# Kernel tuning notes

Measured on AMD Instinct MI355X. Metric: run time of the kernel, lower is better.

The kernel has to match this reference:

```python
import jax, jax.numpy as jnp
import numpy as np

N_SRC = 50000
N_DST = 50000
N_EDGES = 800000
D = 128
H = 128


def setup_inputs() -> dict:
    key = jax.random.key(0)
    ks = jax.random.split(key, 10)
    return {
        "feat_src": jax.random.normal(ks[0], (N_SRC, D), dtype=jnp.float32),
        "feat_dst": jax.random.normal(ks[1], (N_DST, D), dtype=jnp.float32),
        "W1": jax.random.normal(ks[2], (H, D), dtype=jnp.float32) * 0.05,
        "b1": jnp.zeros((H,), dtype=jnp.float32),
        "W2": jax.random.normal(ks[3], (H, 3 * D), dtype=jnp.float32) * 0.05,
        "b2": jnp.zeros((H,), dtype=jnp.float32),
        "W3": jax.random.normal(ks[4], (H, 2 * H), dtype=jnp.float32) * 0.05,
        "b3": jnp.zeros((H,), dtype=jnp.float32),
        "src_idx": jax.random.randint(ks[5], (N_EDGES,), 0, N_SRC, dtype=jnp.int32),
        "dst_idx": jax.random.randint(ks[6], (N_EDGES,), 0, N_DST, dtype=jnp.int32),
    }


def reference(feat_src, feat_dst, W1, b1, W2, b2, W3, b3, src_idx, dst_idx):
    n_dst = feat_dst.shape[0]
    # copy_u: gather source features along edges  [E, D]
    m = feat_src[src_idx]
    # fn.max -> 'max'; NOTE: source code's 'mean' is ALSO fn.max (faithful to bug)
    mx = jax.ops.segment_max(m, dst_idx, num_segments=n_dst)
    mx = jnp.where(jnp.isfinite(mx), mx, jnp.zeros_like(mx))  # zero-degree dst -> 0 (DGL convention)
    sm = jax.ops.segment_sum(m, dst_idx, num_segments=n_dst)
    agg = jnp.concatenate([mx, mx, sm], axis=1)  # [N_dst, 3D]
    z2 = agg @ W2.T + b2            # fc2
    z1 = feat_dst @ W1.T + b1       # fc1
    h = jax.nn.relu(jnp.concatenate([z2, z1], axis=1))  # [N_dst, 2H]
    out = jax.nn.relu(h @ W3.T + b3)  # fc3 = Linear + ReLU
    return out
```

## Files before the change

kernel.cpp:

```cpp
#include <hip/hip_runtime.h>
#include <math.h>

#define NDST 50000
#define NSRC 50000
#define NEDGE 800000
#define DF 128

#define NBUK 1563
#define NCH 128
#define EPC (NEDGE / NCH)
#define HN (NBUK * NCH)
#define CAP 1536

typedef __attribute__((ext_vector_type(4))) float f32x4;
typedef __attribute__((ext_vector_type(8))) short bf16x8;

__device__ __forceinline__ ushort f2bf(float f) {
    union { float f; unsigned int u; } c; c.f = f;
    unsigned int u = c.u;
    unsigned int r = (u + 0x7fffu + ((u >> 16) & 1u)) >> 16;
    return (ushort)r;
}
__device__ __forceinline__ float bflo(unsigned int u) {
    union { unsigned int u; float f; } c; c.u = u << 16; return c.f;
}
__device__ __forceinline__ float bfhi(unsigned int u) {
    union { unsigned int u; float f; } c; c.u = u & 0xffff0000u; return c.f;
}

#define NB_CONV 6250
#define NB_CONVD 6250
#define NB_ZERO 196
#define NB_WF 40

__global__ void prep_all(const float* __restrict__ fs, unsigned int* __restrict__ fs_b,
                         const float* __restrict__ fd, unsigned int* __restrict__ fd_b,
                         uint4* __restrict__ hist4,
                         const float* __restrict__ W2, const float* __restrict__ W1,
                         const float* __restrict__ W3,
                         ushort* __restrict__ Wzf, ushort* __restrict__ W1f,
                         ushort* __restrict__ W3f) {
    int b = blockIdx.x, tid = threadIdx.x;
    if (b < NB_CONV + NB_CONVD) {
        const float* src = (b < NB_CONV) ? fs : fd;
        unsigned int* dst = (b < NB_CONV) ? fs_b : fd_b;
        int i = ((b < NB_CONV) ? b : b - NB_CONV) * 256 + tid;
        float4 v = *(const float4*)(src + (size_t)i * 4);
        unsigned int lo = (unsigned int)f2bf(v.x) | ((unsigned int)f2bf(v.y) << 16);
        unsigned int hi = (unsigned int)f2bf(v.z) | ((unsigned int)f2bf(v.w) << 16);
        *(uint2*)(dst + (size_t)i * 2) = make_uint2(lo, hi);
    } else if (b < NB_CONV + NB_CONVD + NB_ZERO) {
        int i = (b - NB_CONV - NB_CONVD) * 256 + tid;
        if (i < HN / 4) hist4[i] = make_uint4(0, 0, 0, 0);
    } else {
        int i = (b - NB_CONV - NB_CONVD - NB_ZERO) * 256 + tid;
        float v[8];
        ushort* outp;
        if (i < 4096) {
            int e = i, lane = e & 63, nt = (e >> 6) & 7, ks = e >> 9;
            int n = nt * 16 + (lane & 15), kb = ks * 32 + ((lane >> 4) << 3);
            #pragma unroll
            for (int j = 0; j < 8; ++j) {
                int col = kb + j;
                v[j] = (col < 128) ? (W2[n * 384 + col] + W2[n * 384 + 128 + col])
                                   : W2[n * 384 + 128 + col];
            }
            outp = Wzf + (size_t)e * 8;
        } else if (i < 4096 + 2048) {
            int e = i - 4096, lane = e & 63, nt = (e >> 6) & 7, ks = e >> 9;
            int n = nt * 16 + (lane & 15), kb = ks * 32 + ((lane >> 4) << 3);
            #pragma unroll
            for (int j = 0; j < 8; ++j) v[j] = W1[n * 128 + kb + j];
            outp = W1f + (size_t)e * 8;
        } else if (i < 4096 + 2048 + 4096) {
            int e = i - 6144, lane = e & 63, nt = (e >> 6) & 7, ks = e >> 9;
            int n = nt * 16 + (lane & 15), kb = ks * 32 + ((lane >> 4) << 3);
            #pragma unroll
            for (int j = 0; j < 8; ++j) v[j] = W3[n * 256 + kb + j];
            outp = W3f + (size_t)e * 8;
        } else return;
        unsigned int u0 = (unsigned int)f2bf(v[0]) | ((unsigned int)f2bf(v[1]) << 16);
        unsigned int u1 = (unsigned int)f2bf(v[2]) | ((unsigned int)f2bf(v[3]) << 16);
        unsigned int u2 = (unsigned int)f2bf(v[4]) | ((unsigned int)f2bf(v[5]) << 16);
        unsigned int u3 = (unsigned int)f2bf(v[6]) | ((unsigned int)f2bf(v[7]) << 16);
        *(uint4*)outp = make_uint4(u0, u1, u2, u3);
    }
}

__global__ void hist_k(const int* __restrict__ dst_idx, int* __restrict__ hist) {
    int c = blockIdx.x, tid = threadIdx.x;
    int base = c * EPC;
    for (int e = base + tid; e < base + EPC; e += 256)
        atomicAdd(&hist[(dst_idx[e] >> 5) * NCH + c], 1);
}

__global__ void scan_bsums(const int* __restrict__ a, int* __restrict__ bsum, int n) {
    __shared__ int ws[4];
    int i = blockIdx.x * 256 + threadIdx.x;
    int v = (i < n) ? a[i] : 0;
    #pragma unroll
    for (int off = 32; off > 0; off >>= 1) v += __shfl_down(v, off, 64);
    if ((threadIdx.x & 63) == 0) ws[threadIdx.x >> 6] = v;
    __syncthreads();
    if (threadIdx.x == 0) bsum[blockIdx.x] = ws[0] + ws[1] + ws[2] + ws[3];
}

__global__ __launch_bounds__(256)
void scan_mid(const int* __restrict__ bsum, int* __restrict__ bpre, int nb) {
    __shared__ int part[256];
    int t = threadIdx.x;
    int ch = (nb + 255) / 256;
    int lo = t * ch, hi = min(nb, lo + ch);
    int s = 0;
    for (int i = lo; i < hi; ++i) s += bsum[i];
    part[t] = s;
    __syncthreads();
    for (int off = 1; off < 256; off <<= 1) {
        int v = (t >= off) ? part[t - off] : 0;
        __syncthreads();
        part[t] += v;
        __syncthreads();
    }
    int run = (t == 0) ? 0 : part[t - 1];
    for (int i = lo; i < hi; ++i) { bpre[i] = run; run += bsum[i]; }
}

__global__ __launch_bounds__(256)
void scan_final(const int* __restrict__ a, const int* __restrict__ bpre,
                int* __restrict__ out, int n) {
    __shared__ int s[256];
    int b = blockIdx.x, t = threadIdx.x;
    int i = b * 256 + t;
    int v = (i < n) ? a[i] : 0;
    s[t] = v;
    __syncthreads();
    for (int off = 1; off < 256; off <<= 1) {
        int u = (t >= off) ? s[t - off] : 0;
        __syncthreads();
        s[t] += u;
        __syncthreads();
    }
    if (i < n) out[i] = bpre[b] + s[t] - v;
}

__global__ __launch_bounds__(256)
void partition_k(const int* __restrict__ src_idx, const int* __restrict__ dst_idx,
                 const int* __restrict__ scanned, unsigned int* __restrict__ pairs) {
    __shared__ int offs_l[NBUK];
    int c = blockIdx.x, tid = threadIdx.x;
    for (int i = tid; i < NBUK; i += 256) offs_l[i] = scanned[i * NCH + c];
    __syncthreads();
    int base = c * EPC;
    for (int e = base + tid; e < base + EPC; e += 256) {
        int d = dst_idx[e];
        int pos = atomicAdd(&offs_l[d >> 5], 1);
        pairs[pos] = (unsigned int)src_idx[e] | ((unsigned int)(d & 31) << 16);
    }
}

__global__ __launch_bounds__(256)
void bucket_sort_agg(const unsigned int* __restrict__ fs_b,
                     const unsigned int* __restrict__ pairs,
                     const int* __restrict__ scanned,
                     unsigned int* __restrict__ mx_b, unsigned int* __restrict__ sm_b) {
    __shared__ int s_src[CAP];
    __shared__ int s_cnt[32], s_off[32], s_cur[32];
    int B = blockIdx.x, tid = threadIdx.x;
    int w = tid >> 6, lane = tid & 63;
    int s0 = scanned[B * NCH];
    int s1 = (B + 1 < NBUK) ? scanned[(B + 1) * NCH] : NEDGE;

    float mx0[8], mx1[8], sm0[8], sm1[8];
    #pragma unroll
    for (int j = 0; j < 8; ++j) {
        mx0[j] = -INFINITY; mx1[j] = -INFINITY; sm0[j] = 0.f; sm1[j] = 0.f;
    }

    for (int cs = s0; cs < s1; cs += CAP) {
        int n = min(CAP, s1 - cs);
        if (tid < 32) s_cnt[tid] = 0;
        __syncthreads();
        for (int i = tid; i < n; i += 256)
            atomicAdd(&s_cnt[(pairs[cs + i] >> 16) & 31u], 1);
        __syncthreads();
        if (tid < 32) {
            int v = s_cnt[tid];
            int incl = v;
            #pragma unroll
            for (int d = 1; d < 32; d <<= 1) {
                int o = __shfl_up(incl, d, 64);
                if (tid >= d) incl += o;
            }
            s_off[tid] = incl - v;
            s_cur[tid] = incl - v;
        }
        __syncthreads();
        for (int i = tid; i < n; i += 256) {
            unsigned int p = pairs[cs + i];
            int pos = atomicAdd(&s_cur[(p >> 16) & 31u], 1);
            s_src[pos] = (int)(p & 0xFFFFu);
        }
        __syncthreads();
        #pragma unroll
        for (int j = 0; j < 8; ++j) {
            int dl = w * 8 + j;
            int e = s_off[dl], eend = e + s_cnt[dl];
            for (; e + 3 < eend; e += 4) {
                int i0 = s_src[e], i1 = s_src[e + 1], i2 = s_src[e + 2], i3 = s_src[e + 3];
                unsigned int u0 = fs_b[(size_t)i0 * 64 + lane];
                unsigned int u1 = fs_b[(size_t)i1 * 64 + lane];
                unsigned int u2 = fs_b[(size_t)i2 * 64 + lane];
                unsigned int u3 = fs_b[(size_t)i3 * 64 + lane];
                float a0 = bflo(u0), c0 = bfhi(u0);
                float a1 = bflo(u1), c1 = bfhi(u1);
                float a2 = bflo(u2), c2 = bfhi(u2);
                float a3 = bflo(u3), c3 = bfhi(u3);
                mx0[j] = fmaxf(fmaxf(fmaxf(mx0[j], a0), a1), fmaxf(a2, a3));
                mx1[j] = fmaxf(fmaxf(fmaxf(mx1[j], c0), c1), fmaxf(c2, c3));
                sm0[j] += (a0 + a1) + (a2 + a3);
                sm1[j] += (c0 + c1) + (c2 + c3);
            }
            for (; e < eend; ++e) {
                unsigned int u = fs_b[(size_t)s_src[e] * 64 + lane];
                float a = bflo(u), c = bfhi(u);
                mx0[j] = fmaxf(mx0[j], a);
                mx1[j] = fmaxf(mx1[j], c);
                sm0[j] += a;
                sm1[j] += c;
            }
        }
        __syncthreads();
    }

    int base_d = B * 32;
    #pragma unroll
    for (int j = 0; j < 8; ++j) {
        int d = base_d + w * 8 + j;
        if (d >= NDST) continue;
        float m0 = mx0[j], m1 = mx1[j];
        if (m0 == -INFINITY) m0 = 0.f;
        if (m1 == -INFINITY) m1 = 0.f;
        union { float f; unsigned int u; } c0, c1;
        c0.f = m0; c1.f = m1;
        size_t o = (size_t)d * 64 + lane;
        mx_b[o] = (c0.u >> 16) | (c1.u & 0xFFFF0000u);
        sm_b[o] = (unsigned int)f2bf(sm0[j]) | ((unsigned int)f2bf(sm1[j]) << 16);
    }
}

#define BM2 64
#define LDH 260

__global__ __launch_bounds__(256)
void mlp_fused(const ushort* __restrict__ mxa, const ushort* __restrict__ sma,
               const ushort* __restrict__ fdb,
               const ushort* __restrict__ Wzf, const ushort* __restrict__ W1f,
               const ushort* __restrict__ W3f,
               const float* __restrict__ b1, const float* __restrict__ b2,
               const float* __restrict__ b3,
               float* __restrict__ out) {
    __shared__ ushort Hs[BM2 * LDH];
    int tid = threadIdx.x;
    int bm = blockIdx.x * BM2;
    int wid = tid >> 6, lane = tid & 63;
    int wm = (wid & 1) * 32, wn = (wid >> 1) * 64;
    int lrow = lane & 15, lk8 = (lane >> 4) * 8;
    int rbase = (lane >> 4) * 4;
    int nt0 = (wid >> 1) * 4;

    int am0 = min(bm + wm + lrow, NDST - 1);
    int am1 = min(bm + wm + 16 + lrow, NDST - 1);
    int bn[4];
    #pragma unroll
    for (int ni = 0; ni < 4; ++ni) bn[ni] = wn + ni * 16 + lrow;

    f32x4 acc[2][4];

    bf16x8 A0[8], A1[8];
    #pragma unroll
    for (int k = 0; k < 8; ++k) {
        const ushort* ap = (k < 4) ? mxa : sma;
        int kl = ((k * 32) & 127) + lk8;
        A0[k] = *(const bf16x8*)(ap + (size_t)am0 * 128 + kl);
        A1[k] = *(const bf16x8*)(ap + (size_t)am1 * 128 + kl);
    }
    #pragma unroll
    for (int i = 0; i < 2; ++i)
        #pragma unroll
        for (int j = 0; j < 4; ++j) acc[i][j] = (f32x4){0.f, 0.f, 0.f, 0.f};
    #pragma unroll
    for (int k = 0; k < 8; ++k) {
        #pragma unroll
        for (int ni = 0; ni < 4; ++ni) {
            bf16x8 bf = *(const bf16x8*)(Wzf + ((size_t)((k * 8) + nt0 + ni) * 64 + lane) * 8);
            acc[0][ni] = __builtin_amdgcn_mfma_f32_16x16x32_bf16(A0[k], bf, acc[0][ni], 0, 0, 0);
            acc[1][ni] = __builtin_amdgcn_mfma_f32_16x16x32_bf16(A1[k], bf, acc[1][ni], 0, 0, 0);
        }
    }
    #pragma unroll
    for (int ni = 0; ni < 4; ++ni) {
        float bv = b2[bn[ni]];
        #pragma unroll
        for (int mi = 0; mi < 2; ++mi)
            #pragma unroll
            for (int r = 0; r < 4; ++r)
                Hs[(wm + mi * 16 + rbase + r) * LDH + bn[ni]] =
                    f2bf(fmaxf(acc[mi][ni][r] + bv, 0.f));
    }

    bf16x8 B0[4], B1[4];
    #pragma unroll
    for (int k = 0; k < 4; ++k) {
        int kl = k * 32 + lk8;
        B0[k] = *(const bf16x8*)(fdb + (size_t)am0 * 128 + kl);
        B1[k] = *(const bf16x8*)(fdb + (size_t)am1 * 128 + kl);
    }
    #pragma unroll
    for (int i = 0; i < 2; ++i)
        #pragma unroll
        for (int j = 0; j < 4; ++j) acc[i][j] = (f32x4){0.f, 0.f, 0.f, 0.f};
    #pragma unroll
    for (int k = 0; k < 4; ++k) {
        #pragma unroll
        for (int ni = 0; ni < 4; ++ni) {
            bf16x8 bf = *(const bf16x8*)(W1f + ((size_t)((k * 8) + nt0 + ni) * 64 + lane) * 8);
            acc[0][ni] = __builtin_amdgcn_mfma_f32_16x16x32_bf16(B0[k], bf, acc[0][ni], 0, 0, 0);
            acc[1][ni] = __builtin_amdgcn_mfma_f32_16x16x32_bf16(B1[k], bf, acc[1][ni], 0, 0, 0);
        }
    }
    #pragma unroll
    for (int ni = 0; ni < 4; ++ni) {
        float bv = b1[bn[ni]];
        #pragma unroll
        for (int mi = 0; mi < 2; ++mi)
            #pragma unroll
            for (int r = 0; r < 4; ++r)
                Hs[(wm + mi * 16 + rbase + r) * LDH + 128 + bn[ni]] =
                    f2bf(fmaxf(acc[mi][ni][r] + bv, 0.f));
    }

    __syncthreads();

    #pragma unroll
    for (int i = 0; i < 2; ++i)
        #pragma unroll
        for (int j = 0; j < 4; ++j) acc[i][j] = (f32x4){0.f, 0.f, 0.f, 0.f};
    #pragma unroll
    for (int k = 0; k < 8; ++k) {
        bf16x8 af0 = *(const bf16x8*)&Hs[(wm + lrow) * LDH + k * 32 + lk8];
        bf16x8 af1 = *(const bf16x8*)&Hs[(wm + 16 + lrow) * LDH + k * 32 + lk8];
        #pragma unroll
        for (int ni = 0; ni < 4; ++ni) {
            bf16x8 bf = *(const bf16x8*)(W3f + ((size_t)((k * 8) + nt0 + ni) * 64 + lane) * 8);
            acc[0][ni] = __builtin_amdgcn_mfma_f32_16x16x32_bf16(af0, bf, acc[0][ni], 0, 0, 0);
            acc[1][ni] = __builtin_amdgcn_mfma_f32_16x16x32_bf16(af1, bf, acc[1][ni], 0, 0, 0);
        }
    }
    #pragma unroll
    for (int ni = 0; ni < 4; ++ni) {
        float bv = b3[bn[ni]];
        #pragma unroll
        for (int mi = 0; mi < 2; ++mi)
            #pragma unroll
            for (int r = 0; r < 4; ++r) {
                int m = bm + wm + mi * 16 + rbase + r;
                if (m < NDST)
                    out[(size_t)m * 128 + bn[ni]] = fmaxf(acc[mi][ni][r] + bv, 0.f);
            }
    }
}

extern "C" void kernel_launch(void* const* d_in, const int* in_sizes, int n_in,
                              void* d_out, int out_size, void* d_ws, size_t ws_size,
                              hipStream_t stream) {
    const float* feat_src = (const float*)d_in[0];
    const float* feat_dst = (const float*)d_in[1];
    const float* W1 = (const float*)d_in[2];
    const float* b1 = (const float*)d_in[3];
    const float* W2 = (const float*)d_in[4];
    const float* b2 = (const float*)d_in[5];
    const float* W3 = (const float*)d_in[6];
    const float* b3 = (const float*)d_in[7];
    const int* src_idx = (const int*)d_in[8];
    const int* dst_idx = (const int*)d_in[9];

    float* out = (float*)d_out;

    unsigned int* fs_b = (unsigned int*)d_ws;
    unsigned int* mx_b = fs_b + (size_t)NSRC * 64;
    unsigned int* sm_b = mx_b + (size_t)NDST * 64;
    unsigned int* fd_b = sm_b + (size_t)NDST * 64;
    ushort* Wzf = (ushort*)(fd_b + (size_t)NDST * 64);
    ushort* W1f = Wzf + 128 * 256;
    ushort* W3f = W1f + 128 * 128;
    int* hist    = (int*)(W3f + 128 * 256);
    int* scanned = hist + HN;
    int* bsum    = scanned + HN;
    int* bpre    = bsum + 1024;
    unsigned int* pairs = (unsigned int*)(bpre + 1024);

    const int NBH = (HN + 255) / 256;

    prep_all<<<NB_CONV + NB_CONVD + NB_ZERO + NB_WF, 256, 0, stream>>>(
        feat_src, fs_b, feat_dst, fd_b, (uint4*)hist, W2, W1, W3, Wzf, W1f, W3f);

    hist_k<<<NCH, 256, 0, stream>>>(dst_idx, hist);
    scan_bsums<<<NBH, 256, 0, stream>>>(hist, bsum, HN);
    scan_mid<<<1, 256, 0, stream>>>(bsum, bpre, NBH);
    scan_final<<<NBH, 256, 0, stream>>>(hist, bpre, scanned, HN);
    partition_k<<<NCH, 256, 0, stream>>>(src_idx, dst_idx, scanned, pairs);

    bucket_sort_agg<<<NBUK, 256, 0, stream>>>(fs_b, pairs, scanned, mx_b, sm_b);

    mlp_fused<<<(NDST + BM2 - 1) / BM2, 256, 0, stream>>>(
        (const ushort*)mx_b, (const ushort*)sm_b, (const ushort*)fd_b,
        Wzf, W1f, W3f, b1, b2, b3, out);
}
```

Measured before the change: 170.1 us.

## Give each wave its own 16-row strip in fused MLP, removing block sync

The fused MLP kernel now gives each wavefront its own 16 destination rows across all 128 output columns, instead of having four waves share a 64-row tile split into 32x64 pieces. Each wave writes its hidden activations to a private LDS slice, so the block-wide barrier goes away and the padded stride changes to 264. The trade-off is that A operands are loaded once per wave rather than reused across two row sub-tiles. Each wave also reads the full weight matrices, roughly doubling weight traffic per output row through L2.

```diff
diff --git a/kernel.cpp b/kernel.cpp
--- a/kernel.cpp
+++ b/kernel.cpp
@@ -248,8 +248,7 @@
     }
 }
 
-#define BM2 64
-#define LDH 260
+#define LDH 264
 
 __global__ __launch_bounds__(256)
 void mlp_fused(const ushort* __restrict__ mxa, const ushort* __restrict__ sma,
@@ -259,114 +258,83 @@
                const float* __restrict__ b1, const float* __restrict__ b2,
                const float* __restrict__ b3,
                float* __restrict__ out) {
-    __shared__ ushort Hs[BM2 * LDH];
+    __shared__ ushort Hs[4][16 * LDH];
     int tid = threadIdx.x;
-    int bm = blockIdx.x * BM2;
     int wid = tid >> 6, lane = tid & 63;
-    int wm = (wid & 1) * 32, wn = (wid >> 1) * 64;
-    int lrow = lane & 15, lk8 = (lane >> 4) * 8;
+    int mb = (blockIdx.x * 4 + wid) * 16;
+    if (mb >= NDST) return;
+    ushort* hs = &Hs[wid][0];
+
+    int frow = lane & 15;
+    int fk8 = (lane >> 4) * 8;
     int rbase = (lane >> 4) * 4;
-    int nt0 = (wid >> 1) * 4;
-
-    int am0 = min(bm + wm + lrow, NDST - 1);
-    int am1 = min(bm + wm + 16 + lrow, NDST - 1);
-    int bn[4];
-    #pragma unroll
-    for (int ni = 0; ni < 4; ++ni) bn[ni] = wn + ni * 16 + lrow;
-
-    f32x4 acc[2][4];
-
-    bf16x8 A0[8], A1[8];
+
+    f32x4 acc[8];
+
+    bf16x8 A[8];
     #pragma unroll
     for (int k = 0; k < 8; ++k) {
         const ushort* ap = (k < 4) ? mxa : sma;
-        int kl = ((k * 32) & 127) + lk8;
-        A0[k] = *(const bf16x8*)(ap + (size_t)am0 * 128 + kl);
-        A1[k] = *(const bf16x8*)(ap + (size_t)am1 * 128 + kl);
-    }
-    #pragma unroll
-    for (int i = 0; i < 2; ++i)
-        #pragma unroll
-        for (int j = 0; j < 4; ++j) acc[i][j] = (f32x4){0.f, 0.f, 0.f, 0.f};
-    #pragma unroll
-    for (int k = 0; k < 8; ++k) {
-        #pragma unroll
-        for (int ni = 0; ni < 4; ++ni) {
-            bf16x8 bf = *(const bf16x8*)(Wzf + ((size_t)((k * 8) + nt0 + ni) * 64 + lane) * 8);
-            acc[0][ni] = __builtin_amdgcn_mfma_f32_16x16x32_bf16(A0[k], bf, acc[0][ni], 0, 0, 0);
-            acc[1][ni] = __builtin_amdgcn_mfma_f32_16x16x32_bf16(A1[k], bf, acc[1][ni], 0, 0, 0);
-        }
-    }
-    #pragma unroll
-    for (int ni = 0; ni < 4; ++ni) {
-        float bv = b2[bn[ni]];
-        #pragma unroll
-        for (int mi = 0; mi < 2; ++mi)
-            #pragma unroll
-            for (int r = 0; r < 4; ++r)
-                Hs[(wm + mi * 16 + rbase + r) * LDH + bn[ni]] =
-                    f2bf(fmaxf(acc[mi][ni][r] + bv, 0.f));
-    }
-
-    bf16x8 B0[4], B1[4];
-    #pragma unroll
-    for (int k = 0; k < 4; ++k) {
-        int kl = k * 32 + lk8;
-        B0[k] = *(const bf16x8*)(fdb + (size_t)am0 * 128 + kl);
-        B1[k] = *(const bf16x8*)(fdb + (size_t)am1 * 128 + kl);
-    }
-    #pragma unroll
-    for (int i = 0; i < 2; ++i)
-        #pragma unroll
-        for (int j = 0; j < 4; ++j) acc[i][j] = (f32x4){0.f, 0.f, 0.f, 0.f};
-    #pragma unroll
-    for (int k = 0; k < 4; ++k) {
-        #pragma unroll
-        for (int ni = 0; ni < 4; ++ni) {
-            bf16x8 bf = *(const bf16x8*)(W1f + ((size_t)((k * 8) + nt0 + ni) * 64 + lane) * 8);
-            acc[0][ni] = __builtin_amdgcn_mfma_f32_16x16x32_bf16(B0[k], bf, acc[0][ni], 0, 0, 0);
-            acc[1][ni] = __builtin_amdgcn_mfma_f32_16x16x32_bf16(B1[k], bf, acc[1][ni], 0, 0, 0);
-        }
-    }
-    #pragma unroll
-    for (int ni = 0; ni < 4; ++ni) {
-        float bv = b1[bn[ni]];
-        #pragma unroll
-        for (int mi = 0; mi < 2; ++mi)
-            #pragma unroll
-            for (int r = 0; r < 4; ++r)
-                Hs[(wm + mi * 16 + rbase + r) * LDH + 128 + bn[ni]] =
-                    f2bf(fmaxf(acc[mi][ni][r] + bv, 0.f));
-    }
-
-    __syncthreads();
-
-    #pragma unroll
-    for (int i = 0; i < 2; ++i)
-        #pragma unroll
-        for (int j = 0; j < 4; ++j) acc[i][j] = (f32x4){0.f, 0.f, 0.f, 0.f};
-    #pragma unroll
-    for (int k = 0; k < 8; ++k) {
-        bf16x8 af0 = *(const bf16x8*)&Hs[(wm + lrow) * LDH + k * 32 + lk8];
-        bf16x8 af1 = *(const bf16x8*)&Hs[(wm + 16 + lrow) * LDH + k * 32 + lk8];
-        #pragma unroll
-        for (int ni = 0; ni < 4; ++ni) {
-            bf16x8 bf = *(const bf16x8*)(W3f + ((size_t)((k * 8) + nt0 + ni) * 64 + lane) * 8);
-            acc[0][ni] = __builtin_amdgcn_mfma_f32_16x16x32_bf16(af0, bf, acc[0][ni], 0, 0, 0);
-            acc[1][ni] = __builtin_amdgcn_mfma_f32_16x16x32_bf16(af1, bf, acc[1][ni], 0, 0, 0);
-        }
-    }
-    #pragma unroll
-    for (int ni = 0; ni < 4; ++ni) {
-        float bv = b3[bn[ni]];
-        #pragma unroll
-        for (int mi = 0; mi < 2; ++mi)
-            #pragma unroll
-            for (int r = 0; r < 4; ++r) {
-                int m = bm + wm + mi * 16 + rbase + r;
-                if (m < NDST)
-                    out[(size_t)m * 128 + bn[ni]] = fmaxf(acc[mi][ni][r] + bv, 0.f);
-            }
+        A[k] = *(const bf16x8*)(ap + (size_t)(mb + frow) * 128 + ((k * 32) & 127) + fk8);
+    }
+    #pragma unroll
+    for (int nt = 0; nt < 8; ++nt) acc[nt] = (f32x4){0.f, 0.f, 0.f, 0.f};
+    #pragma unroll
+    for (int k = 0; k < 8; ++k)
+        #pragma unroll
+        for (int nt = 0; nt < 8; ++nt) {
+            bf16x8 bf = *(const bf16x8*)(Wzf + ((size_t)(k * 8 + nt) * 64 + lane) * 8);
+            acc[nt] = __builtin_amdgcn_mfma_f32_16x16x32_bf16(A[k], bf, acc[nt], 0, 0, 0);
+        }
+    #pragma unroll
+    for (int nt = 0; nt < 8; ++nt) {
+        float bv = b2[nt * 16 + frow];
+        #pragma unroll
+        for (int r = 0; r < 4; ++r)
+            hs[(rbase + r) * LDH + nt * 16 + frow] = f2bf(fmaxf(acc[nt][r] + bv, 0.f));
+    }
+
+    bf16x8 B[4];
+    #pragma unroll
+    for (int k = 0; k < 4; ++k)
+        B[k] = *(const bf16x8*)(fdb + (size_t)(mb + frow) * 128 + k * 32 + fk8);
+    #pragma unroll
+    for (int nt = 0; nt < 8; ++nt) acc[nt] = (f32x4){0.f, 0.f, 0.f, 0.f};
+    #pragma unroll
+    for (int k = 0; k < 4; ++k)
+        #pragma unroll
+        for (int nt = 0; nt < 8; ++nt) {
+            bf16x8 bf = *(const bf16x8*)(W1f + ((size_t)(k * 8 + nt) * 64 + lane) * 8);
+            acc[nt] = __builtin_amdgcn_mfma_f32_16x16x32_bf16(B[k], bf, acc[nt], 0, 0, 0);
+        }
+    #pragma unroll
+    for (int nt = 0; nt < 8; ++nt) {
+        float bv = b1[nt * 16 + frow];
+        #pragma unroll
+        for (int r = 0; r < 4; ++r)
+            hs[(rbase + r) * LDH + 128 + nt * 16 + frow] = f2bf(fmaxf(acc[nt][r] + bv, 0.f));
+    }
+
+    bf16x8 H[8];
+    #pragma unroll
+    for (int k = 0; k < 8; ++k)
+        H[k] = *(const bf16x8*)&hs[frow * LDH + k * 32 + fk8];
+    #pragma unroll
+    for (int nt = 0; nt < 8; ++nt) acc[nt] = (f32x4){0.f, 0.f, 0.f, 0.f};
+    #pragma unroll
+    for (int k = 0; k < 8; ++k)
+        #pragma unroll
+        for (int nt = 0; nt < 8; ++nt) {
+            bf16x8 bf = *(const bf16x8*)(W3f + ((size_t)(k * 8 + nt) * 64 + lane) * 8);
+            acc[nt] = __builtin_amdgcn_mfma_f32_16x16x32_bf16(H[k], bf, acc[nt], 0, 0, 0);
+        }
+    #pragma unroll
+    for (int nt = 0; nt < 8; ++nt) {
+        float bv = b3[nt * 16 + frow];
+        #pragma unroll
+        for (int r = 0; r < 4; ++r)
+            out[(size_t)(mb + rbase + r) * 128 + nt * 16 + frow] =
+                fmaxf(acc[nt][r] + bv, 0.f);
     }
 }
 
@@ -412,7 +380,7 @@
 
     bucket_sort_agg<<<NBUK, 256, 0, stream>>>(fs_b, pairs, scanned, mx_b, sm_b);
 
-    mlp_fused<<<(NDST + BM2 - 1) / BM2, 256, 0, stream>>>(
+    mlp_fused<<<(NDST / 16 + 3) / 4, 256, 0, stream>>>(
         (const ushort*)mx_b, (const ushort*)sm_b, (const ushort*)fd_b,
         Wzf, W1f, W3f, b1, b2, b3, out);
 }
```

New measurement: 193.0 us. 1.13x slower.
